# Kernel optimization log

Measured on AMD Instinct MI355X. Metric: run time of the kernel, lower is better.

The kernel has to match this reference:

```python
import jax, jax.numpy as jnp
import numpy as np

B = 16384
D = 768           # roberta hidden
SENT = 3          # sentiment features
GRU_IN = D + SENT # 771
H = 128           # memory_dim
FUSION = GRU_IN + H + D  # 1667
E = 7             # num_emotions
S = 65536         # number of (dialog, speaker) memory slots


def setup_inputs() -> dict:
    key = jax.random.key(0)
    ks = jax.random.split(key, 12)
    inp = {
        "h_t": jax.random.normal(ks[0], (B, D), jnp.float32),
        "h_ctx": jax.random.normal(ks[1], (B, D), jnp.float32),
        "sentiment": jax.random.uniform(ks[2], (B, SENT), jnp.float32),
        "slot_ids": jax.random.randint(ks[3], (B,), 0, S, jnp.int32),
        # speaker memory table (gathered/scattered by slot_ids)
        "memory": jax.random.normal(ks[4], (S, H), jnp.float32) * 0.1,
        # GRUCell params (torch layout: rows ordered [r; z; n])
        "W_ih": jax.random.normal(ks[5], (3 * H, GRU_IN), jnp.float32) * 0.02,
        "W_hh": jax.random.normal(ks[6], (3 * H, H), jnp.float32) * 0.02,
        "b_ih": jnp.zeros((3 * H,), jnp.float32),
        "b_hh": jnp.zeros((3 * H,), jnp.float32),
        # heads
        "W_e": jax.random.normal(ks[7], (E, FUSION), jnp.float32) * 0.02,
        "b_e": jnp.zeros((E,), jnp.float32),
        "W_s": jax.random.normal(ks[8], (1, FUSION), jnp.float32) * 0.02,
        "b_s": jnp.zeros((1,), jnp.float32),
    }
    return inp


def _gru_cell(x, h, W_ih, W_hh, b_ih, b_hh):
    # x: [B, GRU_IN], h: [B, H]; torch nn.GRUCell semantics
    gi = x @ W_ih.T + b_ih            # [B, 3H]
    gh = h @ W_hh.T + b_hh            # [B, 3H]
    i_r, i_z, i_n = jnp.split(gi, 3, axis=1)
    h_r, h_z, h_n = jnp.split(gh, 3, axis=1)
    r = jax.nn.sigmoid(i_r + h_r)
    z = jax.nn.sigmoid(i_z + h_z)
    n = jnp.tanh(i_n + r * h_n)
    return (1.0 - z) * n + z * h


def reference(h_t, h_ctx, sentiment, slot_ids, memory, W_ih, W_hh, b_ih, b_hh, W_e, b_e, W_s, b_s):
    h_t_aug = jnp.concatenate([h_t, sentiment], axis=1)      # [B, 771]
    s_t = memory[slot_ids]                                    # gather  [B, H]
    s_new = _gru_cell(h_t_aug, s_t, W_ih, W_hh, b_ih, b_hh)   # [B, H]
    # prediction uses the PRE-update memory s_t (as in the torch loop)
    z_t = jnp.concatenate([h_t_aug, s_t, h_ctx], axis=1)      # [B, 1667] (dropout is identity in eval)
    emotion_logits = z_t @ W_e.T + b_e                        # [B, E]
    shift_logits = (z_t @ W_s.T + b_s)[:, 0]                  # [B]
    # matching the sequential dict updates in the original loop)
    new_memory = memory.at[slot_ids].set(s_new)               # [S, H]
    return emotion_logits, shift_logits, new_memory
```

## Files before the change

kernel.cpp:

```cpp
#include <hip/hip_runtime.h>
#include <hip/hip_bf16.h>

#define B_SZ   16384
#define D_SZ   768
#define H_SZ   128
#define S_SZ   65536
#define E_SZ   7

#define NFR    33
#define NSTEP  53

typedef __attribute__((ext_vector_type(8))) short bf16x8;
typedef __attribute__((ext_vector_type(4))) float f32x4;
typedef __attribute__((ext_vector_type(4))) unsigned int u32x4;

#define LD4(p) (*reinterpret_cast<const float4*>(p))
#define MFMA(d, a, b) d = __builtin_amdgcn_mfma_f32_16x16x32_bf16(a, b, d, 0, 0, 0)

#define GLDS(gp, lp) __builtin_amdgcn_global_load_lds(                              \
        (const __attribute__((address_space(1))) unsigned int*)(gp),                \
        (__attribute__((address_space(3))) unsigned int*)(lp), 16, 0, 0)
#define GLDSN(gp, lp) __builtin_amdgcn_global_load_lds(                             \
        (const __attribute__((address_space(1))) unsigned int*)(gp),                \
        (__attribute__((address_space(3))) unsigned int*)(lp), 16, 0, 2)

#define PIPE_BAR(N) do {                                                            \
        asm volatile("s_waitcnt vmcnt(" #N ")" ::: "memory");                       \
        __builtin_amdgcn_sched_barrier(0);                                          \
        __builtin_amdgcn_s_barrier();                                               \
    } while (0)

static __device__ __forceinline__ ushort f2bf(float v) {
    unsigned u = __float_as_uint(v);
    u = (u + 0x7FFFu + ((u >> 16) & 1u)) >> 16;
    return (ushort)u;
}

static __device__ __forceinline__ unsigned pk2(float x, float y) {
    unsigned a = __float_as_uint(x) + 0x8000u;
    unsigned b = __float_as_uint(y) + 0x8000u;
    return __builtin_amdgcn_perm(b, a, 0x07060302);
}

static __device__ __forceinline__ bf16x8 cvt8(float4 a, float4 b) {
    union { unsigned u[4]; bf16x8 v; } r;
    r.u[0] = pk2(a.x, a.y); r.u[1] = pk2(a.z, a.w);
    r.u[2] = pk2(b.x, b.y); r.u[3] = pk2(b.z, b.w);
    return r.v;
}

static __device__ __forceinline__ float w2_value(int n, int k,
    const float* __restrict__ W_ih, const float* __restrict__ W_hh,
    const float* __restrict__ b_ih, const float* __restrict__ b_hh,
    const float* __restrict__ W_e,  const float* __restrict__ b_e,
    const float* __restrict__ W_s,  const float* __restrict__ b_s)
{
    float v = 0.0f;
    if (n < 256) {
        if (k < 768)                        v = W_ih[(size_t)n * 771 + k];
        else if (k < 896)                   v = W_hh[(size_t)n * 128 + (k - 768)];
        else if (k >= 1664 && k < 1667)     v = W_ih[(size_t)n * 771 + 768 + (k - 1664)];
        else if (k == 1667)                 v = b_ih[n] + b_hh[n];
    } else if (n < 384) {
        if (k < 768)                        v = W_ih[(size_t)n * 771 + k];
        else if (k >= 1664 && k < 1667)     v = W_ih[(size_t)n * 771 + 768 + (k - 1664)];
        else if (k == 1667)                 v = b_ih[n];
    } else if (n < 512) {
        int g = n - 128;
        if (k >= 768 && k < 896)            v = W_hh[(size_t)g * 128 + (k - 768)];
        else if (k == 1667)                 v = b_hh[g];
    } else if (n < 520) {
        int e = n - 512;
        const float* Wr = (e < E_SZ) ? (W_e + (size_t)e * 1667) : W_s;
        if (k < 768)                        v = Wr[k];
        else if (k < 896)                   v = Wr[771 + (k - 768)];
        else if (k < 1664)                  v = Wr[899 + (k - 896)];
        else if (k < 1667)                  v = Wr[768 + (k - 1664)];
        else if (k == 1667)                 v = (e < E_SZ) ? b_e[e] : b_s[0];
    }
    return v;
}

__global__ __launch_bounds__(256) void pack_w2f_kernel(
    const float* __restrict__ W_ih, const float* __restrict__ W_hh,
    const float* __restrict__ b_ih, const float* __restrict__ b_hh,
    const float* __restrict__ W_e,  const float* __restrict__ b_e,
    const float* __restrict__ W_s,  const float* __restrict__ b_s,
    ushort* __restrict__ W2f)
{
    int tid = blockIdx.x * 256 + threadIdx.x;
    if (tid >= NFR * NSTEP * 64) return;
    int lane  = tid & 63;
    int kstep = (tid >> 6) % NSTEP;
    int nf    = tid / (NSTEP * 64);
    int n     = nf * 16 + (lane & 15);
    int kbase = kstep * 32 + (lane >> 4) * 8;
    ushort o[8];
#pragma unroll
    for (int j = 0; j < 8; ++j)
        o[j] = f2bf(w2_value(n, kbase + j, W_ih, W_hh, b_ih, b_hh, W_e, b_e, W_s, b_s));
    *reinterpret_cast<uint4*>(W2f + (size_t)tid * 8) = *reinterpret_cast<const uint4*>(o);
}

__global__ __launch_bounds__(256) void winner_kernel(const int* __restrict__ slot_ids,
                                                     int* __restrict__ winner)
{
    int b = blockIdx.x * 256 + threadIdx.x;
    if (b < B_SZ) atomicMax(&winner[slot_ids[b]], b);
}

static __device__ __forceinline__ bf16x8 ldB(const ushort* __restrict__ W2f, int nf, int ks, int lane) {
    return *reinterpret_cast<const bf16x8*>(W2f + ((size_t)(nf * NSTEP + ks) * 64 + lane) * 8);
}

static __device__ __forceinline__ float4 lds_rd(const char* Ab, int st, int row, int h) {
    return *reinterpret_cast<const float4*>(Ab + st * 2048 + row * 128 + ((h ^ (row & 7)) << 4));
}

template<int W>
static __device__ __forceinline__ void ht4(int c, const char* Ab, int lane,
                                           const ushort* __restrict__ W2f,
                                           f32x4* __restrict__ acc, f32x4* __restrict__ hacc)
{
    const int cl = lane & 15, kg = lane >> 4;
#pragma unroll
    for (int st = 0; st < 4; ++st) {
        const int s = c * 4 + st;
        bf16x8 B0 = ldB(W2f, W, s, lane), B1 = ldB(W2f, 8 + W, s, lane), B2 = ldB(W2f, 16 + W, s, lane);
        float4 x0 = lds_rd(Ab, st, cl, 2 * kg), x1 = lds_rd(Ab, st, cl, 2 * kg + 1);
        bf16x8 a0 = cvt8(x0, x1);
        MFMA(acc[0], a0, B0); MFMA(acc[1], a0, B1); MFMA(acc[2], a0, B2);
        if ((s & 7) == W) {
            bf16x8 Bh = ldB(W2f, 32, s, lane);
            MFMA(hacc[0], a0, Bh);
        }
    }
}

template<int W>
static __device__ __forceinline__ void st4(const char* Ab, int lane,
                                           const ushort* __restrict__ W2f,
                                           f32x4* __restrict__ acc, f32x4* __restrict__ hacc)
{
    const int cl = lane & 15, kg = lane >> 4;
#pragma unroll
    for (int t = 0; t < 4; ++t) {
        const int s = 24 + t;
        bf16x8 B0 = ldB(W2f, W, s, lane), B1 = ldB(W2f, 8 + W, s, lane), B2 = ldB(W2f, 24 + W, s, lane);
        float4 x0 = lds_rd(Ab, t, cl, 2 * kg), x1 = lds_rd(Ab, t, cl, 2 * kg + 1);
        bf16x8 a0 = cvt8(x0, x1);
        MFMA(acc[0], a0, B0); MFMA(acc[1], a0, B1); MFMA(acc[3], a0, B2);
        if constexpr (W < 4) {
            if (t == W) {
                bf16x8 Bh = ldB(W2f, 32, s, lane);
                MFMA(hacc[0], a0, Bh);
            }
        }
    }
}

template<int W>
static __device__ __forceinline__ void ctx4(int c, const char* Ab, int lane,
                                            const ushort* __restrict__ W2f,
                                            f32x4* __restrict__ hacc)
{
    if ((c & 1) == (W >> 2)) {
        const int cl = lane & 15, kg = lane >> 4;
        const int st = W & 3;
        const int s  = c * 4 + st;
        bf16x8 Bh = ldB(W2f, 32, s, lane);
        float4 x0 = lds_rd(Ab, st, cl, 2 * kg), x1 = lds_rd(Ab, st, cl, 2 * kg + 1);
        MFMA(hacc[0], cvt8(x0, x1), Bh);
    }
}

template<int W>
static __device__ __forceinline__ void tail_and_gru(
    const float* __restrict__ sent, const float* __restrict__ memory,
    const int* __restrict__ slot_ids, const int* __restrict__ winner,
    int row0, int lane, const ushort* __restrict__ W2f,
    f32x4* __restrict__ acc, f32x4* __restrict__ hacc, float* __restrict__ out_mem)
{
    const int cl = lane & 15, kg = lane >> 4;
    {
        const int rA0 = row0 + cl;
        bf16x8 a0;
#pragma unroll
        for (int jj = 0; jj < 8; ++jj) {
            int kk = kg * 8 + jj;
            float v0 = 0.f;
            if (kk < 3)       v0 = sent[(size_t)rA0 * 3 + kk];
            else if (kk == 3) v0 = 1.f;
            a0[jj] = (short)f2bf(v0);
        }
        bf16x8 T0 = ldB(W2f, W, 52, lane),      T1 = ldB(W2f, 8 + W, 52, lane);
        bf16x8 T2 = ldB(W2f, 16 + W, 52, lane), T3 = ldB(W2f, 24 + W, 52, lane);
        MFMA(acc[0], a0, T0); MFMA(acc[1], a0, T1);
        MFMA(acc[2], a0, T2); MFMA(acc[3], a0, T3);
        if constexpr (W == 4) {
            bf16x8 Bh = ldB(W2f, 32, 52, lane);
            MFMA(hacc[0], a0, Bh);
        }
    }
    const int j = 16 * W + cl;
#pragma unroll
    for (int rr = 0; rr < 4; ++rr) {
        const int row  = row0 + kg * 4 + rr;
        const int slot = slot_ids[row];
        const bool win = (winner[slot] == row);
        float rgate = acc[0][rr];
        float zg    = acc[1][rr];
        float inn   = acc[2][rr];
        float hnn   = acc[3][rr];
        rgate = 1.0f / (1.0f + __expf(-rgate));
        zg    = 1.0f / (1.0f + __expf(-zg));
        float nn = tanhf(inn + rgate * hnn);
        float h  = memory[(size_t)slot * H_SZ + j];
        float sn = (1.0f - zg) * nn + zg * h;
        if (win) out_mem[(size_t)slot * H_SZ + j] = sn;
    }
}

__global__ __launch_bounds__(512, 8) void fused_kernel(
    const float* __restrict__ h_t,   const float* __restrict__ h_ctx,
    const float* __restrict__ sent,  const int* __restrict__ slot_ids,
    const float* __restrict__ memory,const ushort* __restrict__ W2f,
    const int* __restrict__ winner,
    float* __restrict__ out_emo, float* __restrict__ out_shift, float* __restrict__ out_mem)
{
    __shared__ alignas(16) char  A_st[3][4 * 2048];
    __shared__ alignas(16) f32x4 redh[8 * 64];

    const int tid  = threadIdx.x;
    const int wave = tid >> 6;
    const int lane = tid & 63;
    const int row0 = blockIdx.x * 16;

    const int sst   = wave >> 1;
    const int sbh   = (wave & 1) * 1024;
    const int srow  = (wave & 1) * 8 + (lane >> 3);
    const int scg   = (lane & 7) ^ (srow & 7);
    const int sslot = slot_ids[row0 + srow];

    f32x4 acc[4], hacc[1];
    {
        f32x4 z = {0.f, 0.f, 0.f, 0.f};
#pragma unroll
        for (int i = 0; i < 4; ++i) acc[i] = z;
        hacc[0] = z;
    }

#define STAGE(C) do {                                                                     \
        const int s_ = 4 * (C) + sst;                                                     \
        char* dst_ = &A_st[(C) % 3][sst * 2048 + sbh];                                    \
        if (s_ < 24)      GLDSN(h_t + (size_t)(row0 + srow) * D_SZ + s_ * 32 + scg * 4, dst_); \
        else if (s_ < 28) GLDS(memory + (size_t)sslot * H_SZ + (s_ - 24) * 32 + scg * 4, dst_); \
        else              GLDSN(h_ctx + (size_t)(row0 + srow) * D_SZ + (s_ - 28) * 32 + scg * 4, dst_); \
    } while (0)

#define COPYSL(I0) do {                                                                   \
        int idx  = (I0) * 512 + tid;                           \
        int rr   = idx >> 5;                                          \
        int c4   = (idx & 31) * 4;                                                        \
        int slot = blockIdx.x * 64 + rr;                                                  \
        if (winner[slot] < 0) {                                                           \
            u32x4 v = __builtin_nontemporal_load(                                         \
                reinterpret_cast<const u32x4*>(memory + (size_t)slot * H_SZ + c4));       \
            __builtin_nontemporal_store(v,                                                \
                reinterpret_cast<u32x4*>(out_mem + (size_t)slot * H_SZ + c4));            \
        } } while (0)

#define BYWAVE(...) do { switch (wave) {                                                  \
    case 0: { constexpr int W = 0; __VA_ARGS__; } break;                                  \
    case 1: { constexpr int W = 1; __VA_ARGS__; } break;                                  \
    case 2: { constexpr int W = 2; __VA_ARGS__; } break;                                  \
    case 3: { constexpr int W = 3; __VA_ARGS__; } break;                                  \
    case 4: { constexpr int W = 4; __VA_ARGS__; } break;                                  \
    case 5: { constexpr int W = 5; __VA_ARGS__; } break;                                  \
    case 6: { constexpr int W = 6; __VA_ARGS__; } break;                                  \
    default:{ constexpr int W = 7; __VA_ARGS__; } break; } } while (0)

    STAGE(0); STAGE(1);
    PIPE_BAR(1);

    BYWAVE(ht4<W>(0, A_st[0], lane, W2f, acc, hacc)); COPYSL(0); STAGE(2);  PIPE_BAR(1);
    BYWAVE(ht4<W>(1, A_st[1], lane, W2f, acc, hacc)); COPYSL(1); STAGE(3);  PIPE_BAR(1);
    BYWAVE(ht4<W>(2, A_st[2], lane, W2f, acc, hacc)); COPYSL(2); STAGE(4);  PIPE_BAR(1);
    BYWAVE(ht4<W>(3, A_st[0], lane, W2f, acc, hacc)); COPYSL(3); STAGE(5);  PIPE_BAR(1);
    BYWAVE(ht4<W>(4, A_st[1], lane, W2f, acc, hacc));            STAGE(6);  PIPE_BAR(1);
    BYWAVE(ht4<W>(5, A_st[2], lane, W2f, acc, hacc));            STAGE(7);  PIPE_BAR(1);
    BYWAVE(st4<W>(A_st[0], lane, W2f, acc, hacc));               STAGE(8);  PIPE_BAR(1);
    BYWAVE(ctx4<W>(7,  A_st[1], lane, W2f, hacc));               STAGE(9);  PIPE_BAR(1);
    BYWAVE(ctx4<W>(8,  A_st[2], lane, W2f, hacc));               STAGE(10); PIPE_BAR(1);
    BYWAVE(ctx4<W>(9,  A_st[0], lane, W2f, hacc));               STAGE(11); PIPE_BAR(1);
    BYWAVE(ctx4<W>(10, A_st[1], lane, W2f, hacc));               STAGE(12); PIPE_BAR(1);
    BYWAVE(ctx4<W>(11, A_st[2], lane, W2f, hacc));                          PIPE_BAR(0);
    BYWAVE((ctx4<W>(12, A_st[0], lane, W2f, hacc),
            tail_and_gru<W>(sent, memory, slot_ids, winner, row0, lane, W2f,
                            acc, hacc, out_mem)));

    __syncthreads();
    redh[wave * 64 + lane] = hacc[0];
    __syncthreads();
    if (tid < 64) {
        f32x4 hv = redh[tid];
#pragma unroll
        for (int w = 1; w < 8; ++w) hv += redh[w * 64 + tid];
        const int col  = tid & 15;
        const int rowb = row0 + (tid >> 4) * 4;
#pragma unroll
        for (int rr = 0; rr < 4; ++rr) {
            const int row = rowb + rr;
            if (col < E_SZ)       out_emo[(size_t)row * E_SZ + col] = hv[rr];
            else if (col == E_SZ) out_shift[row] = hv[rr];
        }
    }
#undef STAGE
#undef COPYSL
#undef BYWAVE
}

extern "C" void kernel_launch(void* const* d_in, const int* in_sizes, int n_in,
                              void* d_out, int out_size, void* d_ws, size_t ws_size,
                              hipStream_t stream)
{
    const float* h_t     = (const float*)d_in[0];
    const float* h_ctx   = (const float*)d_in[1];
    const float* sent    = (const float*)d_in[2];
    const int*   slot_ids= (const int*)  d_in[3];
    const float* memory  = (const float*)d_in[4];
    const float* W_ih    = (const float*)d_in[5];
    const float* W_hh    = (const float*)d_in[6];
    const float* b_ih    = (const float*)d_in[7];
    const float* b_hh    = (const float*)d_in[8];
    const float* W_e     = (const float*)d_in[9];
    const float* b_e     = (const float*)d_in[10];
    const float* W_s     = (const float*)d_in[11];
    const float* b_s     = (const float*)d_in[12];

    float* out       = (float*)d_out;
    float* out_emo   = out;
    float* out_shift = out + (size_t)B_SZ * E_SZ;
    float* out_mem   = out + (size_t)B_SZ * E_SZ + B_SZ;

    int*    winner = (int*)d_ws;
    ushort* W2f    = (ushort*)((char*)d_ws + (size_t)S_SZ * sizeof(int));

    hipMemsetAsync(winner, 0xFF, (size_t)S_SZ * sizeof(int), stream);

    pack_w2f_kernel<<<(NFR * NSTEP * 64 + 255) / 256, 256, 0, stream>>>(
        W_ih, W_hh, b_ih, b_hh, W_e, b_e, W_s, b_s, W2f);
    winner_kernel<<<B_SZ / 256, 256, 0, stream>>>(slot_ids, winner);
    fused_kernel<<<B_SZ / 16, 512, 0, stream>>>(
        h_t, h_ctx, sent, slot_ids, memory, W2f, winner, out_emo, out_shift, out_mem);
}
```

Baseline: 84.34 us.

## Process 32 rows per block to reuse each weight fragment across two M-tiles

Each block now handles 32 rows instead of 16. Every wave runs two 16-row MFMA tiles that share the same B (weight) fragments, which halves how often weights are loaded from global memory per row. The staging buffers, accumulators, reduction buffer, COPYSL coverage and grid size are doubled or halved to match, and occupancy in launch bounds drops from 8 to 4. This trades extra register and LDS pressure, plus fewer resident blocks, for half the weight traffic.

```diff
diff --git a/kernel.cpp b/kernel.cpp
--- a/kernel.cpp
+++ b/kernel.cpp
@@ -114,7 +114,7 @@
 }
 
 static __device__ __forceinline__ float4 lds_rd(const char* Ab, int st, int row, int h) {
-    return *reinterpret_cast<const float4*>(Ab + st * 2048 + row * 128 + ((h ^ (row & 7)) << 4));
+    return *reinterpret_cast<const float4*>(Ab + st * 4096 + row * 128 + ((h ^ (row & 7)) << 4));
 }
 
 template<int W>
@@ -130,9 +130,12 @@
         float4 x0 = lds_rd(Ab, st, cl, 2 * kg), x1 = lds_rd(Ab, st, cl, 2 * kg + 1);
         bf16x8 a0 = cvt8(x0, x1);
         MFMA(acc[0], a0, B0); MFMA(acc[1], a0, B1); MFMA(acc[2], a0, B2);
+        float4 y0 = lds_rd(Ab, st, 16 + cl, 2 * kg), y1 = lds_rd(Ab, st, 16 + cl, 2 * kg + 1);
+        bf16x8 a1 = cvt8(y0, y1);
+        MFMA(acc[4], a1, B0); MFMA(acc[5], a1, B1); MFMA(acc[6], a1, B2);
         if ((s & 7) == W) {
             bf16x8 Bh = ldB(W2f, 32, s, lane);
-            MFMA(hacc[0], a0, Bh);
+            MFMA(hacc[0], a0, Bh); MFMA(hacc[1], a1, Bh);
         }
     }
 }
@@ -150,10 +153,13 @@
         float4 x0 = lds_rd(Ab, t, cl, 2 * kg), x1 = lds_rd(Ab, t, cl, 2 * kg + 1);
         bf16x8 a0 = cvt8(x0, x1);
         MFMA(acc[0], a0, B0); MFMA(acc[1], a0, B1); MFMA(acc[3], a0, B2);
+        float4 y0 = lds_rd(Ab, t, 16 + cl, 2 * kg), y1 = lds_rd(Ab, t, 16 + cl, 2 * kg + 1);
+        bf16x8 a1 = cvt8(y0, y1);
+        MFMA(acc[4], a1, B0); MFMA(acc[5], a1, B1); MFMA(acc[7], a1, B2);
         if constexpr (W < 4) {
             if (t == W) {
                 bf16x8 Bh = ldB(W2f, 32, s, lane);
-                MFMA(hacc[0], a0, Bh);
+                MFMA(hacc[0], a0, Bh); MFMA(hacc[1], a1, Bh);
             }
         }
     }
@@ -171,6 +177,8 @@
         bf16x8 Bh = ldB(W2f, 32, s, lane);
         float4 x0 = lds_rd(Ab, st, cl, 2 * kg), x1 = lds_rd(Ab, st, cl, 2 * kg + 1);
         MFMA(hacc[0], cvt8(x0, x1), Bh);
+        float4 y0 = lds_rd(Ab, st, 16 + cl, 2 * kg), y1 = lds_rd(Ab, st, 16 + cl, 2 * kg + 1);
+        MFMA(hacc[1], cvt8(y0, y1), Bh);
     }
 }
 
@@ -183,86 +191,93 @@
 {
     const int cl = lane & 15, kg = lane >> 4;
     {
-        const int rA0 = row0 + cl;
-        bf16x8 a0;
+        const int rA0 = row0 + cl, rA1 = rA0 + 16;
+        bf16x8 a0, a1;
 #pragma unroll
         for (int jj = 0; jj < 8; ++jj) {
             int kk = kg * 8 + jj;
-            float v0 = 0.f;
-            if (kk < 3)       v0 = sent[(size_t)rA0 * 3 + kk];
-            else if (kk == 3) v0 = 1.f;
-            a0[jj] = (short)f2bf(v0);
+            float v0 = 0.f, v1 = 0.f;
+            if (kk < 3)       { v0 = sent[(size_t)rA0 * 3 + kk]; v1 = sent[(size_t)rA1 * 3 + kk]; }
+            else if (kk == 3) { v0 = 1.f; v1 = 1.f; }
+            a0[jj] = (short)f2bf(v0); a1[jj] = (short)f2bf(v1);
         }
         bf16x8 T0 = ldB(W2f, W, 52, lane),      T1 = ldB(W2f, 8 + W, 52, lane);
         bf16x8 T2 = ldB(W2f, 16 + W, 52, lane), T3 = ldB(W2f, 24 + W, 52, lane);
         MFMA(acc[0], a0, T0); MFMA(acc[1], a0, T1);
         MFMA(acc[2], a0, T2); MFMA(acc[3], a0, T3);
+        MFMA(acc[4], a1, T0); MFMA(acc[5], a1, T1);
+        MFMA(acc[6], a1, T2); MFMA(acc[7], a1, T3);
         if constexpr (W == 4) {
             bf16x8 Bh = ldB(W2f, 32, 52, lane);
-            MFMA(hacc[0], a0, Bh);
+            MFMA(hacc[0], a0, Bh); MFMA(hacc[1], a1, Bh);
         }
     }
     const int j = 16 * W + cl;
 #pragma unroll
-    for (int rr = 0; rr < 4; ++rr) {
-        const int row  = row0 + kg * 4 + rr;
-        const int slot = slot_ids[row];
-        const bool win = (winner[slot] == row);
-        float rgate = acc[0][rr];
-        float zg    = acc[1][rr];
-        float inn   = acc[2][rr];
-        float hnn   = acc[3][rr];
-        rgate = 1.0f / (1.0f + __expf(-rgate));
-        zg    = 1.0f / (1.0f + __expf(-zg));
-        float nn = tanhf(inn + rgate * hnn);
-        float h  = memory[(size_t)slot * H_SZ + j];
-        float sn = (1.0f - zg) * nn + zg * h;
-        if (win) out_mem[(size_t)slot * H_SZ + j] = sn;
-    }
-}
-
-__global__ __launch_bounds__(512, 8) void fused_kernel(
+    for (int rg = 0; rg < 2; ++rg) {
+#pragma unroll
+        for (int rr = 0; rr < 4; ++rr) {
+            const int row  = row0 + rg * 16 + kg * 4 + rr;
+            const int slot = slot_ids[row];
+            const bool win = (winner[slot] == row);
+            float rgate = acc[rg * 4 + 0][rr];
+            float zg    = acc[rg * 4 + 1][rr];
+            float inn   = acc[rg * 4 + 2][rr];
+            float hnn   = acc[rg * 4 + 3][rr];
+            rgate = 1.0f / (1.0f + __expf(-rgate));
+            zg    = 1.0f / (1.0f + __expf(-zg));
+            float nn = tanhf(inn + rgate * hnn);
+            float h  = memory[(size_t)slot * H_SZ + j];
+            float sn = (1.0f - zg) * nn + zg * h;
+            if (win) out_mem[(size_t)slot * H_SZ + j] = sn;
+        }
+    }
+}
+
+__global__ __launch_bounds__(512, 4) void fused_kernel(
     const float* __restrict__ h_t,   const float* __restrict__ h_ctx,
     const float* __restrict__ sent,  const int* __restrict__ slot_ids,
     const float* __restrict__ memory,const ushort* __restrict__ W2f,
     const int* __restrict__ winner,
     float* __restrict__ out_emo, float* __restrict__ out_shift, float* __restrict__ out_mem)
 {
-    __shared__ alignas(16) char  A_st[3][4 * 2048];
-    __shared__ alignas(16) f32x4 redh[8 * 64];
+    __shared__ alignas(16) char  A_st[3][4 * 4096];
+    __shared__ alignas(16) f32x4 redh[2][8 * 64];
 
     const int tid  = threadIdx.x;
     const int wave = tid >> 6;
     const int lane = tid & 63;
-    const int row0 = blockIdx.x * 16;
-
-    const int sst   = wave >> 1;
-    const int sbh   = (wave & 1) * 1024;
-    const int srow  = (wave & 1) * 8 + (lane >> 3);
+    const int row0 = blockIdx.x * 32;
+
+    const int sst   = wave >> 2;
+    const int srb   = wave & 3;
+    const int srow  = srb * 8 + (lane >> 3);
     const int scg   = (lane & 7) ^ (srow & 7);
     const int sslot = slot_ids[row0 + srow];
 
-    f32x4 acc[4], hacc[1];
+    f32x4 acc[8], hacc[2];
     {
         f32x4 z = {0.f, 0.f, 0.f, 0.f};
 #pragma unroll
-        for (int i = 0; i < 4; ++i) acc[i] = z;
-        hacc[0] = z;
-    }
-
-#define STAGE(C) do {                                                                     \
-        const int s_ = 4 * (C) + sst;                                                     \
-        char* dst_ = &A_st[(C) % 3][sst * 2048 + sbh];                                    \
-        if (s_ < 24)      GLDSN(h_t + (size_t)(row0 + srow) * D_SZ + s_ * 32 + scg * 4, dst_); \
-        else if (s_ < 28) GLDS(memory + (size_t)sslot * H_SZ + (s_ - 24) * 32 + scg * 4, dst_); \
+        for (int i = 0; i < 8; ++i) acc[i] = z;
+        hacc[0] = z; hacc[1] = z;
+    }
+
+#define STAGE(C) do { _Pragma("unroll")                                                   \
+    for (int q = 0; q < 2; ++q) {                                                         \
+        const int st_ = sst + 2 * q;                                                      \
+        const int s_  = 4 * (C) + st_;                                                    \
+        char* dst_ = &A_st[(C) % 3][st_ * 4096 + srb * 1024];                             \
+        if (s_ < 24)      GLDSN(h_t + (size_t)(row0 + srow) * D_SZ + s_ * 32 + scg * 4, dst_);          \
+        else if (s_ < 28) GLDS(memory + (size_t)sslot * H_SZ + (s_ - 24) * 32 + scg * 4, dst_);         \
         else              GLDSN(h_ctx + (size_t)(row0 + srow) * D_SZ + (s_ - 28) * 32 + scg * 4, dst_); \
-    } while (0)
+    } } while (0)
 
 #define COPYSL(I0) do {                                                                   \
         int idx  = (I0) * 512 + tid;                           \
-        int rr   = idx >> 5;                                          \
+        int rr   = idx >> 5;                                         \
         int c4   = (idx & 31) * 4;                                                        \
-        int slot = blockIdx.x * 64 + rr;                                                  \
+        int slot = blockIdx.x * 128 + rr;                                                 \
         if (winner[slot] < 0) {                                                           \
             u32x4 v = __builtin_nontemporal_load(                                         \
                 reinterpret_cast<const u32x4*>(memory + (size_t)slot * H_SZ + c4));       \
@@ -281,33 +296,35 @@
     default:{ constexpr int W = 7; __VA_ARGS__; } break; } } while (0)
 
     STAGE(0); STAGE(1);
-    PIPE_BAR(1);
-
-    BYWAVE(ht4<W>(0, A_st[0], lane, W2f, acc, hacc)); COPYSL(0); STAGE(2);  PIPE_BAR(1);
-    BYWAVE(ht4<W>(1, A_st[1], lane, W2f, acc, hacc)); COPYSL(1); STAGE(3);  PIPE_BAR(1);
-    BYWAVE(ht4<W>(2, A_st[2], lane, W2f, acc, hacc)); COPYSL(2); STAGE(4);  PIPE_BAR(1);
-    BYWAVE(ht4<W>(3, A_st[0], lane, W2f, acc, hacc)); COPYSL(3); STAGE(5);  PIPE_BAR(1);
-    BYWAVE(ht4<W>(4, A_st[1], lane, W2f, acc, hacc));            STAGE(6);  PIPE_BAR(1);
-    BYWAVE(ht4<W>(5, A_st[2], lane, W2f, acc, hacc));            STAGE(7);  PIPE_BAR(1);
-    BYWAVE(st4<W>(A_st[0], lane, W2f, acc, hacc));               STAGE(8);  PIPE_BAR(1);
-    BYWAVE(ctx4<W>(7,  A_st[1], lane, W2f, hacc));               STAGE(9);  PIPE_BAR(1);
-    BYWAVE(ctx4<W>(8,  A_st[2], lane, W2f, hacc));               STAGE(10); PIPE_BAR(1);
-    BYWAVE(ctx4<W>(9,  A_st[0], lane, W2f, hacc));               STAGE(11); PIPE_BAR(1);
-    BYWAVE(ctx4<W>(10, A_st[1], lane, W2f, hacc));               STAGE(12); PIPE_BAR(1);
+    PIPE_BAR(2);
+
+    BYWAVE(ht4<W>(0, A_st[0], lane, W2f, acc, hacc)); COPYSL(0); STAGE(2);  PIPE_BAR(2);
+    BYWAVE(ht4<W>(1, A_st[1], lane, W2f, acc, hacc)); COPYSL(1); STAGE(3);  PIPE_BAR(2);
+    BYWAVE(ht4<W>(2, A_st[2], lane, W2f, acc, hacc)); COPYSL(2); STAGE(4);  PIPE_BAR(2);
+    BYWAVE(ht4<W>(3, A_st[0], lane, W2f, acc, hacc)); COPYSL(3); STAGE(5);  PIPE_BAR(2);
+    BYWAVE(ht4<W>(4, A_st[1], lane, W2f, acc, hacc)); COPYSL(4); STAGE(6);  PIPE_BAR(2);
+    BYWAVE(ht4<W>(5, A_st[2], lane, W2f, acc, hacc)); COPYSL(5); STAGE(7);  PIPE_BAR(2);
+    BYWAVE(st4<W>(A_st[0], lane, W2f, acc, hacc));    COPYSL(6); STAGE(8);  PIPE_BAR(2);
+    BYWAVE(ctx4<W>(7,  A_st[1], lane, W2f, hacc));    COPYSL(7); STAGE(9);  PIPE_BAR(2);
+    BYWAVE(ctx4<W>(8,  A_st[2], lane, W2f, hacc));               STAGE(10); PIPE_BAR(2);
+    BYWAVE(ctx4<W>(9,  A_st[0], lane, W2f, hacc));               STAGE(11); PIPE_BAR(2);
+    BYWAVE(ctx4<W>(10, A_st[1], lane, W2f, hacc));               STAGE(12); PIPE_BAR(2);
     BYWAVE(ctx4<W>(11, A_st[2], lane, W2f, hacc));                          PIPE_BAR(0);
     BYWAVE((ctx4<W>(12, A_st[0], lane, W2f, hacc),
             tail_and_gru<W>(sent, memory, slot_ids, winner, row0, lane, W2f,
                             acc, hacc, out_mem)));
 
     __syncthreads();
-    redh[wave * 64 + lane] = hacc[0];
+    redh[0][wave * 64 + lane] = hacc[0];
+    redh[1][wave * 64 + lane] = hacc[1];
     __syncthreads();
-    if (tid < 64) {
-        f32x4 hv = redh[tid];
-#pragma unroll
-        for (int w = 1; w < 8; ++w) hv += redh[w * 64 + tid];
-        const int col  = tid & 15;
-        const int rowb = row0 + (tid >> 4) * 4;
+    if (tid < 128) {
+        const int rg = tid >> 6, l = tid & 63;
+        f32x4 hv = redh[rg][l];
+#pragma unroll
+        for (int w = 1; w < 8; ++w) hv += redh[rg][w * 64 + l];
+        const int col  = l & 15;
+        const int rowb = row0 + rg * 16 + (l >> 4) * 4;
 #pragma unroll
         for (int rr = 0; rr < 4; ++rr) {
             const int row = rowb + rr;
@@ -351,6 +368,6 @@
     pack_w2f_kernel<<<(NFR * NSTEP * 64 + 255) / 256, 256, 0, stream>>>(
         W_ih, W_hh, b_ih, b_hh, W_e, b_e, W_s, b_s, W2f);
     winner_kernel<<<B_SZ / 256, 256, 0, stream>>>(slot_ids, winner);
-    fused_kernel<<<B_SZ / 16, 512, 0, stream>>>(
+    fused_kernel<<<B_SZ / 32, 512, 0, stream>>>(
         h_t, h_ctx, sent, slot_ids, memory, W2f, winner, out_emo, out_shift, out_mem);
 }
```

New measurement: 70.14 us. 1.2x faster.
